# Kernel optimization log

Hardware: AMD Instinct MI355X
Metric: run time of the kernel (lower is better)

## Reference

```python
import jax, jax.numpy as jnp
import numpy as np

B, T, V, E, H, C = 64, 512, 32000, 256, 512, 4

def setup_inputs() -> dict:
    key = jax.random.key(0)
    ks = jax.random.split(key, 8)
    s = 1.0 / np.sqrt(H)  # torch LSTM default init scale
    return {
        "x": jax.random.randint(ks[0], (B, T), 0, V),
        "emb": jax.random.normal(ks[1], (V, E), jnp.float32) * 0.1,
        "W_ih": jax.random.uniform(ks[2], (4 * H, E), jnp.float32, -s, s),
        "W_hh": jax.random.uniform(ks[3], (4 * H, H), jnp.float32, -s, s),
        "b_ih": jax.random.uniform(ks[4], (4 * H,), jnp.float32, -s, s),
        "b_hh": jax.random.uniform(ks[5], (4 * H,), jnp.float32, -s, s),
        "W_fc": jax.random.uniform(ks[6], (C, H), jnp.float32, -s, s),
        "b_fc": jax.random.uniform(ks[7], (C,), jnp.float32, -s, s),
    }

def _lstm_last_hidden(e, W_ih, W_hh, b_ih, b_hh):
    # e: [B,T,E]. Precompute input-side gate preactivations for all steps.
    xg = jnp.einsum('bte,ge->tbg', e, W_ih) + (b_ih + b_hh)  # [T,B,4H]
    h0 = jnp.zeros((e.shape[0], H), e.dtype)
    c0 = jnp.zeros((e.shape[0], H), e.dtype)

    def step(carry, xt):
        h, c = carry
        g = xt + h @ W_hh.T                       # [B,4H]
        i, f, gg, o = jnp.split(g, 4, axis=-1)    # torch gate order: i,f,g,o
        i = jax.nn.sigmoid(i)
        f = jax.nn.sigmoid(f)
        gg = jnp.tanh(gg)
        o = jax.nn.sigmoid(o)
        c = f * c + i * gg
        h = o * jnp.tanh(c)
        return (h, c), None

    (hT, _), _ = jax.lax.scan(step, (h0, c0), xg)
    return hT  # last hidden == lstm_out[:, -1, :] for unidirectional LSTM

def reference(x, emb, W_ih, W_hh, b_ih, b_hh, W_fc, b_fc):
    e = emb[x]                                    # [B,T,E] embedding lookup
    hT = _lstm_last_hidden(e, W_ih, W_hh, b_ih, b_hh)
    return hT @ W_fc.T + b_fc                     # [B,C] logits
```

## Files before the change

kernel.cpp:

```cpp
#include <hip/hip_runtime.h>
#include <hip/hip_bf16.h>

#define B_  64
#define T_  512
#define E_  256
#define H_  512
#define G4_ 2048
#define C_  4

typedef __attribute__((ext_vector_type(4))) float  f32x4;
typedef __attribute__((ext_vector_type(8))) __bf16 bf16x8;
typedef __attribute__((ext_vector_type(8))) short  short8;
typedef __attribute__((ext_vector_type(4))) short  s16x4;

union V16 { f32x4 f; bf16x8 b; short8 s; };

__device__ __forceinline__ float sigmoid_(float x) { return 1.0f / (1.0f + __expf(-x)); }
__device__ __forceinline__ float tanh_(float x)    { return 1.0f - 2.0f / (__expf(2.0f * x) + 1.0f); }

__device__ __forceinline__ short f2bf(float f) {
  union { float f; unsigned u; } v; v.f = f;
  return (short)((v.u + 0x7FFFu + ((v.u >> 16) & 1u)) >> 16);
}

__device__ __forceinline__ void store_short_llc(void* p, unsigned v) {
  asm volatile("global_store_short %0, %1, off sc0 sc1" :: "v"(p), "v"(v) : "memory");
}
__device__ __forceinline__ void store_dword_llc(void* p, float v) {
  asm volatile("global_store_dword %0, %1, off sc0 sc1" :: "v"(p), "v"(v) : "memory");
}
__device__ __forceinline__ f32x4 ld_b128_llc(const void* p) {
  f32x4 v;
  asm volatile("global_load_dwordx4 %0, %1, off sc0 sc1\n\ts_waitcnt vmcnt(0)"
               : "=&v"(v) : "v"(p) : "memory");
  return v;
}

__global__ __launch_bounds__(256, 1) void wih_conv(const float* __restrict__ W,
                                                   short* __restrict__ out) {
  const int i = (blockIdx.x * 256 + threadIdx.x) * 4;
  f32x4 v = *(const f32x4*)(W + i);
  s16x4 s;
  s[0] = f2bf(v[0]); s[1] = f2bf(v[1]); s[2] = f2bf(v[2]); s[3] = f2bf(v[3]);
  *(s16x4*)(out + i) = s;
}

union XgSmem {
  struct { int idx[B_]; short e[B_][E_ + 8]; } g;
  short o[4][64][136];
};

template<bool WBF16>
__global__ __launch_bounds__(256, 2) void xg_kernel(
    const int* __restrict__ x, const float* __restrict__ emb,
    const void* __restrict__ Wv,
    __hip_bfloat16* __restrict__ xg)
{
  const int t   = blockIdx.x;
  const int tid = threadIdx.x;
  __shared__ XgSmem sm;

  if (tid < B_) sm.g.idx[tid] = x[tid * T_ + t];
  __syncthreads();
  {
    int b = tid >> 2, ch = tid & 3;
    const float* src = emb + (size_t)sm.g.idx[b] * E_ + ch * 64;
    short* dst = &sm.g.e[b][ch * 64];
#pragma unroll
    for (int i = 0; i < 16; i++) {
      f32x4 v = *(const f32x4*)(src + i * 4);
      s16x4 s;
      s[0] = f2bf(v[0]); s[1] = f2bf(v[1]); s[2] = f2bf(v[2]); s[3] = f2bf(v[3]);
      *(s16x4*)(dst + i * 4) = s;
    }
  }
  __syncthreads();

  const int wv   = tid >> 6;
  const int lane = tid & 63;
  const int ln15 = lane & 15, quad = lane >> 4;

  V16 breg[4][8];
#pragma unroll
  for (int nt = 0; nt < 4; nt++)
#pragma unroll
    for (int ks = 0; ks < 8; ks++)
      breg[nt][ks].f = *(const f32x4*)(&sm.g.e[nt * 16 + ln15][quad * 8 + ks * 32]);
  __syncthreads();

  const int gbase = wv * 512;
  const size_t base_t = (size_t)t * (G4_ * B_);

  for (int q = 0; q < 4; q++) {
#pragma unroll
    for (int m8 = 0; m8 < 8; m8++) {
      const int mt = q * 8 + m8;
      V16 areg[8];
      if constexpr (WBF16) {
        const short* arow = (const short*)Wv + (size_t)(gbase + mt * 16 + ln15) * E_ + quad * 8;
#pragma unroll
        for (int ks = 0; ks < 8; ks++)
          areg[ks].f = *(const f32x4*)(arow + ks * 32);
      } else {
        const float* arow = (const float*)Wv + (size_t)(gbase + mt * 16 + ln15) * E_ + quad * 8;
#pragma unroll
        for (int ks = 0; ks < 8; ks++) {
          f32x4 lo = *(const f32x4*)(arow + ks * 32);
          f32x4 hi = *(const f32x4*)(arow + ks * 32 + 4);
          short8 s;
          s[0] = f2bf(lo[0]); s[1] = f2bf(lo[1]); s[2] = f2bf(lo[2]); s[3] = f2bf(lo[3]);
          s[4] = f2bf(hi[0]); s[5] = f2bf(hi[1]); s[6] = f2bf(hi[2]); s[7] = f2bf(hi[3]);
          areg[ks].s = s;
        }
      }

      f32x4 acc[4];
#pragma unroll
      for (int nt = 0; nt < 4; nt++) acc[nt] = (f32x4){0.f, 0.f, 0.f, 0.f};
#pragma unroll
      for (int ks = 0; ks < 8; ks++)
#pragma unroll
        for (int nt = 0; nt < 4; nt++)
          acc[nt] = __builtin_amdgcn_mfma_f32_16x16x32_bf16(areg[ks].b, breg[nt][ks].b, acc[nt], 0, 0, 0);

      const int dl = m8 * 16 + quad * 4;
#pragma unroll
      for (int nt = 0; nt < 4; nt++) {
        const int batch = nt * 16 + ln15;
        s16x4 sv;
#pragma unroll
        for (int r = 0; r < 4; r++) sv[r] = f2bf(acc[nt][r]);
        *(s16x4*)&sm.o[wv][batch][dl] = sv;
      }
    }

    const size_t qbase = base_t + ((size_t)wv << 15) + q * 128;
    const int chunk = lane & 15;
#pragma unroll
    for (int i = 0; i < 16; i++) {
      const int row = (lane >> 4) + i * 4;
      f32x4 v = *(const f32x4*)&sm.o[wv][row][chunk * 8];
      *(f32x4*)((short*)xg + qbase + ((size_t)row << 9) + chunk * 8) = v;
    }
  }
}

__global__ __launch_bounds__(512, 2) void lstm_kernel(
    const float* __restrict__ W_hh,
    const float* __restrict__ b_ih, const float* __restrict__ b_hh,
    const float* __restrict__ W_fc, const float* __restrict__ b_fc,
    const __hip_bfloat16* __restrict__ xg,
    unsigned int* flags, __hip_bfloat16* hbuf , float* hT,
    float* out)
{
  const int tid  = threadIdx.x;
  const int blk  = blockIdx.x;
  const int g    = blk & 7;
  const int pd   = blk >> 3;
  const int d0   = pd * 64;
  const int wv   = tid >> 6;
  const int lane = tid & 63;
  const int ln15 = lane & 15, quad = lane >> 4;

  __shared__ __hip_bfloat16 s_h[16][520];
  __shared__ float s_pre[4][8][68];

  const int gate  = wv >> 1;
  const int dhalf = (wv & 1) * 32;
  V16 areg[2][16];
#pragma unroll
  for (int tau = 0; tau < 2; tau++) {
    const int grow = gate * 512 + d0 + dhalf + tau * 16 + ln15;
    const float* ap = W_hh + (size_t)grow * H_ + quad * 8;
#pragma unroll
    for (int ks = 0; ks < 16; ks++) {
      f32x4 lo = *(const f32x4*)(ap + ks * 32);
      f32x4 hi = *(const f32x4*)(ap + ks * 32 + 4);
      short8 s;
      s[0] = f2bf(lo[0]); s[1] = f2bf(lo[1]); s[2] = f2bf(lo[2]); s[3] = f2bf(lo[3]);
      s[4] = f2bf(hi[0]); s[5] = f2bf(hi[1]); s[6] = f2bf(hi[2]); s[7] = f2bf(hi[3]);
      areg[tau][ks].s = s;
    }
  }

  const int nb = tid >> 6;
  const int nd = tid & 63;
  const int gb = g * 8 + nb;
  const int dg = d0 + nd;
  const float bias_i = b_ih[dg]        + b_hh[dg];
  const float bias_f = b_ih[512 + dg]  + b_hh[512 + dg];
  const float bias_g = b_ih[1024 + dg] + b_hh[1024 + dg];
  const float bias_o = b_ih[1536 + dg] + b_hh[1536 + dg];
  float c = 0.0f;
  const int myflag = g * 16 + pd;

  *(f32x4*)&s_h[8 + (tid >> 6)][(tid & 63) * 8] = (f32x4){0.f, 0.f, 0.f, 0.f};

  for (int t = 0; t < T_; t++) {
    const int cur = t & 1, nxt = cur ^ 1;

    const size_t xoff = (size_t)t * (G4_ * B_) + ((size_t)gb << 9) + dg;
    const __hip_bfloat16 xgi = xg[xoff];
    const __hip_bfloat16 xgf = xg[xoff + (1u << 15)];
    const __hip_bfloat16 xgg = xg[xoff + (2u << 15)];
    const __hip_bfloat16 xgo = xg[xoff + (3u << 15)];

    if (tid < 8) {
      const unsigned* fp = flags + g * 16 + tid;
      while (__hip_atomic_load(fp, __ATOMIC_RELAXED, __HIP_MEMORY_SCOPE_AGENT) < (unsigned)t) {}
    }
    __syncthreads();

    {
      const short* hbase = (const short*)hbuf + (size_t)cur * (B_ * H_) + (size_t)(g * 8) * H_;
      f32x4 va = ld_b128_llc(hbase + tid * 8);
      *(f32x4*)&s_h[tid >> 6][(tid & 63) * 8] = va;
    }
    __syncthreads();

    f32x4 acc0 = (f32x4){0.f, 0.f, 0.f, 0.f};
    f32x4 acc1 = (f32x4){0.f, 0.f, 0.f, 0.f};
#pragma unroll
    for (int ks = 0; ks < 16; ks++) {
      V16 b0;
      b0.f = *(const f32x4*)&s_h[ln15][quad * 8 + ks * 32];
      acc0 = __builtin_amdgcn_mfma_f32_16x16x32_bf16(areg[0][ks].b, b0.b, acc0, 0, 0, 0);
      acc1 = __builtin_amdgcn_mfma_f32_16x16x32_bf16(areg[1][ks].b, b0.b, acc1, 0, 0, 0);
    }

    if (ln15 < 8) {
      *(f32x4*)&s_pre[gate][ln15][dhalf + quad * 4]      = acc0;
      *(f32x4*)&s_pre[gate][ln15][dhalf + 16 + quad * 4] = acc1;
    }
    __syncthreads();

    {
      const float pi = s_pre[0][nb][nd] + bias_i + __bfloat162float(xgi);
      const float pf = s_pre[1][nb][nd] + bias_f + __bfloat162float(xgf);
      const float pg = s_pre[2][nb][nd] + bias_g + __bfloat162float(xgg);
      const float po = s_pre[3][nb][nd] + bias_o + __bfloat162float(xgo);
      const float i_ = sigmoid_(pi), f_ = sigmoid_(pf);
      const float g_ = tanh_(pg),    o_ = sigmoid_(po);
      c = f_ * c + i_ * g_;
      const float h = o_ * tanh_(c);
      if (t < T_ - 1) {
        store_short_llc((short*)hbuf + (size_t)nxt * (B_ * H_) + (size_t)gb * H_ + dg,
                        (unsigned)(unsigned short)f2bf(h));
      } else {
        store_dword_llc(hT + gb * H_ + dg, h);
      }
    }
    __syncthreads();

    if (tid == 0)
      __hip_atomic_store(&flags[myflag], (unsigned)(t + 1),
                         __ATOMIC_RELAXED, __HIP_MEMORY_SCOPE_AGENT);
  }

  if (blk == 0) {
    if (tid < 64)
      while (__hip_atomic_load(flags + (tid >> 3) * 16 + (tid & 7),
                               __ATOMIC_RELAXED, __HIP_MEMORY_SCOPE_AGENT) < (unsigned)T_) {}
    __builtin_amdgcn_fence(__ATOMIC_ACQUIRE, "agent");
    __syncthreads();
    for (int o = tid; o < B_ * C_; o += 512) {
      const int b = o >> 2, cl = o & 3;
      const f32x4* hr = (const f32x4*)(hT + b * H_);
      const f32x4* wr = (const f32x4*)(W_fc + cl * H_);
      float s = 0.f;
      for (int d4 = 0; d4 < H_ / 4; d4++) {
        const f32x4 hv = hr[d4];
        const f32x4 wv4 = wr[d4];
        s += hv[0] * wv4[0] + hv[1] * wv4[1] + hv[2] * wv4[2] + hv[3] * wv4[3];
      }
      s += b_fc[cl];
      out[o] = s;
    }
  }
}

extern "C" void kernel_launch(void* const* d_in, const int* in_sizes, int n_in,
                              void* d_out, int out_size, void* d_ws, size_t ws_size,
                              hipStream_t stream) {
  const int*   x    = (const int*)d_in[0];
  const float* emb  = (const float*)d_in[1];
  const float* W_ih = (const float*)d_in[2];
  const float* W_hh = (const float*)d_in[3];
  const float* b_ih = (const float*)d_in[4];
  const float* b_hh = (const float*)d_in[5];
  const float* W_fc = (const float*)d_in[6];
  const float* b_fc = (const float*)d_in[7];
  float* out = (float*)d_out;

  char* ws = (char*)d_ws;
  const size_t XG_OFF  = 524288;
  const size_t XG_END  = XG_OFF + (size_t)T_ * G4_ * B_ * 2;
  const size_t NEEDED2 = XG_END + (size_t)G4_ * E_ * 2;
  if (ws_size < XG_END) return;

  unsigned int*   flags = (unsigned int*)ws;
  __hip_bfloat16* hbuf  = (__hip_bfloat16*)(ws + 4096);
  float*          hT    = (float*)(ws + 135168);
  __hip_bfloat16* xg    = (__hip_bfloat16*)(ws + XG_OFF);
  short*          wih16 = (short*)(ws + XG_END);

  (void)hipMemsetAsync(ws, 0, 135168, stream);

  if (ws_size >= NEEDED2) {
    wih_conv<<<512, 256, 0, stream>>>(W_ih, wih16);
    xg_kernel<true><<<T_, 256, 0, stream>>>(x, emb, wih16, xg);
  } else {
    xg_kernel<false><<<T_, 256, 0, stream>>>(x, emb, W_ih, xg);
  }
  lstm_kernel<<<64, 512, 0, stream>>>(W_hh, b_ih, b_hh, W_fc, b_fc, xg,
                                      flags, hbuf, hT, out);
}
```

Measured before the change: 1.263 ms.

## Replace per-step flag barriers with step-tagged hidden-state words and in-register gate math

Each hidden value is now stored as a 32-bit word that packs the step number with the bf16 value, so consumers spin on the data itself rather than on separate per-block flags. This drops the flag polling, the flag store and two block barriers per timestep. W_hh rows are reordered so each MFMA output lane holds all four gates for one unit, which lets the cell update run in registers without the shared-memory pre-activation exchange. The next step's xg values are prefetched, and a double-buffered LDS copy of h replaces one barrier. In exchange the hbuf traffic doubles in size, and every lane polls with repeated 128-bit loads, which adds load on the L2.

```diff
diff --git a/kernel.cpp b/kernel.cpp
--- a/kernel.cpp
+++ b/kernel.cpp
@@ -23,17 +23,17 @@
   return (short)((v.u + 0x7FFFu + ((v.u >> 16) & 1u)) >> 16);
 }
 
-__device__ __forceinline__ void store_short_llc(void* p, unsigned v) {
-  asm volatile("global_store_short %0, %1, off sc0 sc1" :: "v"(p), "v"(v) : "memory");
-}
-__device__ __forceinline__ void store_dword_llc(void* p, float v) {
+__device__ __forceinline__ void store_dword_llc_f(void* p, float v) {
   asm volatile("global_store_dword %0, %1, off sc0 sc1" :: "v"(p), "v"(v) : "memory");
 }
-__device__ __forceinline__ f32x4 ld_b128_llc(const void* p) {
-  f32x4 v;
-  asm volatile("global_load_dwordx4 %0, %1, off sc0 sc1\n\ts_waitcnt vmcnt(0)"
-               : "=&v"(v) : "v"(p) : "memory");
-  return v;
+__device__ __forceinline__ void store_dword_llc_u(void* p, unsigned v) {
+  asm volatile("global_store_dword %0, %1, off sc0 sc1" :: "v"(p), "v"(v) : "memory");
+}
+__device__ __forceinline__ void ld2_b128_llc(const void* p, f32x4& a, f32x4& b) {
+  asm volatile("global_load_dwordx4 %0, %2, off sc0 sc1\n\t"
+               "global_load_dwordx4 %1, %2, off offset:16 sc0 sc1\n\t"
+               "s_waitcnt vmcnt(0)"
+               : "=&v"(a), "=&v"(b) : "v"(p) : "memory");
 }
 
 __global__ __launch_bounds__(256, 1) void wih_conv(const float* __restrict__ W,
@@ -150,7 +150,7 @@
     const float* __restrict__ b_ih, const float* __restrict__ b_hh,
     const float* __restrict__ W_fc, const float* __restrict__ b_fc,
     const __hip_bfloat16* __restrict__ xg,
-    unsigned int* flags, __hip_bfloat16* hbuf , float* hT,
+    unsigned int* flags, unsigned int* hbuf , float* hT,
     float* out)
 {
   const int tid  = threadIdx.x;
@@ -162,15 +162,12 @@
   const int lane = tid & 63;
   const int ln15 = lane & 15, quad = lane >> 4;
 
-  __shared__ __hip_bfloat16 s_h[16][520];
-  __shared__ float s_pre[4][8][68];
-
-  const int gate  = wv >> 1;
-  const int dhalf = (wv & 1) * 32;
+  __shared__ __hip_bfloat16 s_h[2][16][520];
+
   V16 areg[2][16];
 #pragma unroll
   for (int tau = 0; tau < 2; tau++) {
-    const int grow = gate * 512 + d0 + dhalf + tau * 16 + ln15;
+    const int grow = (ln15 & 3) * 512 + d0 + wv * 8 + tau * 4 + (ln15 >> 2);
     const float* ap = W_hh + (size_t)grow * H_ + quad * 8;
 #pragma unroll
     for (int ks = 0; ks < 16; ks++) {
@@ -183,38 +180,61 @@
     }
   }
 
-  const int nb = tid >> 6;
-  const int nd = tid & 63;
-  const int gb = g * 8 + nb;
-  const int dg = d0 + nd;
-  const float bias_i = b_ih[dg]        + b_hh[dg];
-  const float bias_f = b_ih[512 + dg]  + b_hh[512 + dg];
-  const float bias_g = b_ih[1024 + dg] + b_hh[1024 + dg];
-  const float bias_o = b_ih[1536 + dg] + b_hh[1536 + dg];
-  float c = 0.0f;
-  const int myflag = g * 16 + pd;
-
-  *(f32x4*)&s_h[8 + (tid >> 6)][(tid & 63) * 8] = (f32x4){0.f, 0.f, 0.f, 0.f};
+  const int gb_ = g * 8 + ln15;
+  float bias[2][4];
+  float cst[2] = {0.f, 0.f};
+  __hip_bfloat16 xv[2][4];
+  if (ln15 < 8) {
+#pragma unroll
+    for (int tau = 0; tau < 2; tau++) {
+      const int dg_ = d0 + wv * 8 + tau * 4 + quad;
+#pragma unroll
+      for (int gg = 0; gg < 4; gg++)
+        bias[tau][gg] = b_ih[gg * 512 + dg_] + b_hh[gg * 512 + dg_];
+    }
+    const size_t xb = ((size_t)gb_ << 9);
+#pragma unroll
+    for (int tau = 0; tau < 2; tau++) {
+      const int dg_ = d0 + wv * 8 + tau * 4 + quad;
+#pragma unroll
+      for (int gg = 0; gg < 4; gg++)
+        xv[tau][gg] = xg[xb + ((size_t)gg << 15) + dg_];
+    }
+  }
+
+  *(f32x4*)&s_h[0][8 + wv][lane * 8] = (f32x4){0.f, 0.f, 0.f, 0.f};
+  *(f32x4*)&s_h[1][8 + wv][lane * 8] = (f32x4){0.f, 0.f, 0.f, 0.f};
+
+  const unsigned* hb0 = hbuf + ((size_t)(g * 8) << 9) + tid * 8;
+  const unsigned* hb1 = hb0 + B_ * H_;
+  unsigned* sb0 = hbuf + ((size_t)gb_ << 9);
+  unsigned* sb1 = sb0 + B_ * H_;
 
   for (int t = 0; t < T_; t++) {
-    const int cur = t & 1, nxt = cur ^ 1;
-
-    const size_t xoff = (size_t)t * (G4_ * B_) + ((size_t)gb << 9) + dg;
-    const __hip_bfloat16 xgi = xg[xoff];
-    const __hip_bfloat16 xgf = xg[xoff + (1u << 15)];
-    const __hip_bfloat16 xgg = xg[xoff + (2u << 15)];
-    const __hip_bfloat16 xgo = xg[xoff + (3u << 15)];
-
-    if (tid < 8) {
-      const unsigned* fp = flags + g * 16 + tid;
-      while (__hip_atomic_load(fp, __ATOMIC_RELAXED, __HIP_MEMORY_SCOPE_AGENT) < (unsigned)t) {}
-    }
-    __syncthreads();
-
     {
-      const short* hbase = (const short*)hbuf + (size_t)cur * (B_ * H_) + (size_t)(g * 8) * H_;
-      f32x4 va = ld_b128_llc(hbase + tid * 8);
-      *(f32x4*)&s_h[tid >> 6][(tid & 63) * 8] = va;
+      const unsigned want = (unsigned)t;
+      const unsigned* hb = (t & 1) ? hb1 : hb0;
+      f32x4 va, vb;
+      for (;;) {
+        ld2_b128_llc(hb, va, vb);
+        unsigned bad = 0;
+#pragma unroll
+        for (int i = 0; i < 4; i++) {
+          bad |= (__float_as_uint(va[i]) >> 16) ^ want;
+          bad |= (__float_as_uint(vb[i]) >> 16) ^ want;
+        }
+        if (!bad) break;
+      }
+      short8 sv;
+      sv[0] = (short)(__float_as_uint(va[0]) & 0xffffu);
+      sv[1] = (short)(__float_as_uint(va[1]) & 0xffffu);
+      sv[2] = (short)(__float_as_uint(va[2]) & 0xffffu);
+      sv[3] = (short)(__float_as_uint(va[3]) & 0xffffu);
+      sv[4] = (short)(__float_as_uint(vb[0]) & 0xffffu);
+      sv[5] = (short)(__float_as_uint(vb[1]) & 0xffffu);
+      sv[6] = (short)(__float_as_uint(vb[2]) & 0xffffu);
+      sv[7] = (short)(__float_as_uint(vb[3]) & 0xffffu);
+      *(short8*)&s_h[t & 1][tid >> 6][(tid & 63) * 8] = sv;
     }
     __syncthreads();
 
@@ -223,44 +243,55 @@
 #pragma unroll
     for (int ks = 0; ks < 16; ks++) {
       V16 b0;
-      b0.f = *(const f32x4*)&s_h[ln15][quad * 8 + ks * 32];
+      b0.f = *(const f32x4*)&s_h[t & 1][ln15][quad * 8 + ks * 32];
       acc0 = __builtin_amdgcn_mfma_f32_16x16x32_bf16(areg[0][ks].b, b0.b, acc0, 0, 0, 0);
       acc1 = __builtin_amdgcn_mfma_f32_16x16x32_bf16(areg[1][ks].b, b0.b, acc1, 0, 0, 0);
     }
 
     if (ln15 < 8) {
-      *(f32x4*)&s_pre[gate][ln15][dhalf + quad * 4]      = acc0;
-      *(f32x4*)&s_pre[gate][ln15][dhalf + 16 + quad * 4] = acc1;
-    }
-    __syncthreads();
-
-    {
-      const float pi = s_pre[0][nb][nd] + bias_i + __bfloat162float(xgi);
-      const float pf = s_pre[1][nb][nd] + bias_f + __bfloat162float(xgf);
-      const float pg = s_pre[2][nb][nd] + bias_g + __bfloat162float(xgg);
-      const float po = s_pre[3][nb][nd] + bias_o + __bfloat162float(xgo);
-      const float i_ = sigmoid_(pi), f_ = sigmoid_(pf);
-      const float g_ = tanh_(pg),    o_ = sigmoid_(po);
-      c = f_ * c + i_ * g_;
-      const float h = o_ * tanh_(c);
-      if (t < T_ - 1) {
-        store_short_llc((short*)hbuf + (size_t)nxt * (B_ * H_) + (size_t)gb * H_ + dg,
-                        (unsigned)(unsigned short)f2bf(h));
-      } else {
-        store_dword_llc(hT + gb * H_ + dg, h);
-      }
-    }
-    __syncthreads();
-
-    if (tid == 0)
-      __hip_atomic_store(&flags[myflag], (unsigned)(t + 1),
-                         __ATOMIC_RELAXED, __HIP_MEMORY_SCOPE_AGENT);
-  }
+      unsigned* sb = (t & 1) ? sb0 : sb1;
+#pragma unroll
+      for (int tau = 0; tau < 2; tau++) {
+        const f32x4 a = tau ? acc1 : acc0;
+        const float pi = a[0] + bias[tau][0] + __bfloat162float(xv[tau][0]);
+        const float pf = a[1] + bias[tau][1] + __bfloat162float(xv[tau][1]);
+        const float pg = a[2] + bias[tau][2] + __bfloat162float(xv[tau][2]);
+        const float po = a[3] + bias[tau][3] + __bfloat162float(xv[tau][3]);
+        const float i_ = sigmoid_(pi), f_ = sigmoid_(pf);
+        const float g_ = tanh_(pg),    o_ = sigmoid_(po);
+        cst[tau] = f_ * cst[tau] + i_ * g_;
+        const float h = o_ * tanh_(cst[tau]);
+        const int dg_ = d0 + wv * 8 + tau * 4 + quad;
+        if (t < T_ - 1) {
+          const unsigned pw = ((unsigned)(t + 1) << 16) | (unsigned)(unsigned short)f2bf(h);
+          store_dword_llc_u(sb + dg_, pw);
+        } else {
+          store_dword_llc_f(hT + gb_ * H_ + dg_, h);
+        }
+      }
+      if (t + 1 < T_) {
+        const size_t xb = (size_t)(t + 1) * (G4_ * B_) + ((size_t)gb_ << 9);
+#pragma unroll
+        for (int tau = 0; tau < 2; tau++) {
+          const int dg_ = d0 + wv * 8 + tau * 4 + quad;
+#pragma unroll
+          for (int gg = 0; gg < 4; gg++)
+            xv[tau][gg] = xg[xb + ((size_t)gg << 15) + dg_];
+        }
+      }
+    }
+  }
+
+  asm volatile("s_waitcnt vmcnt(0)" ::: "memory");
+  __syncthreads();
+  if (tid == 0)
+    __hip_atomic_store(&flags[g * 16 + pd], 1u,
+                       __ATOMIC_RELAXED, __HIP_MEMORY_SCOPE_AGENT);
 
   if (blk == 0) {
     if (tid < 64)
       while (__hip_atomic_load(flags + (tid >> 3) * 16 + (tid & 7),
-                               __ATOMIC_RELAXED, __HIP_MEMORY_SCOPE_AGENT) < (unsigned)T_) {}
+                               __ATOMIC_RELAXED, __HIP_MEMORY_SCOPE_AGENT) < 1u) {}
     __builtin_amdgcn_fence(__ATOMIC_ACQUIRE, "agent");
     __syncthreads();
     for (int o = tid; o < B_ * C_; o += 512) {
@@ -299,12 +330,12 @@
   if (ws_size < XG_END) return;
 
   unsigned int*   flags = (unsigned int*)ws;
-  __hip_bfloat16* hbuf  = (__hip_bfloat16*)(ws + 4096);
-  float*          hT    = (float*)(ws + 135168);
+  unsigned int*   hbuf  = (unsigned int*)(ws + 4096);
+  float*          hT    = (float*)(ws + 266240);
   __hip_bfloat16* xg    = (__hip_bfloat16*)(ws + XG_OFF);
   short*          wih16 = (short*)(ws + XG_END);
 
-  (void)hipMemsetAsync(ws, 0, 135168, stream);
+  (void)hipMemsetAsync(ws, 0, 266240, stream);
 
   if (ws_size >= NEEDED2) {
     wih_conv<<<512, 256, 0, stream>>>(W_ih, wih16);
```

After: 2.233 ms. 76.8% more time.

## Interleave gate rows in MFMA tiles to do cell update in registers

Applied to the files above, without the earlier changes.

Reorders the W_hh rows loaded into each wave's MFMA A-operand so that each 16-row tile holds the i,f,g,o gates for 4 hidden units side by side. Each lane's accumulator then already contains all four gate preactivations for one (batch, unit) pair. This removes the shared-memory staging buffer for preactivations and one block-wide barrier per timestep on the serial recurrence path. In exchange, only half the lanes (ln15<8) do the pointwise math, each handling two units, and the xg loads become scattered per lane.

```diff
diff --git a/kernel.cpp b/kernel.cpp
--- a/kernel.cpp
+++ b/kernel.cpp
@@ -163,14 +163,11 @@
   const int ln15 = lane & 15, quad = lane >> 4;
 
   __shared__ __hip_bfloat16 s_h[16][520];
-  __shared__ float s_pre[4][8][68];
-
-  const int gate  = wv >> 1;
-  const int dhalf = (wv & 1) * 32;
+
   V16 areg[2][16];
 #pragma unroll
   for (int tau = 0; tau < 2; tau++) {
-    const int grow = gate * 512 + d0 + dhalf + tau * 16 + ln15;
+    const int grow = (ln15 & 3) * 512 + d0 + wv * 8 + tau * 4 + (ln15 >> 2);
     const float* ap = W_hh + (size_t)grow * H_ + quad * 8;
 #pragma unroll
     for (int ks = 0; ks < 16; ks++) {
@@ -183,27 +180,37 @@
     }
   }
 
-  const int nb = tid >> 6;
-  const int nd = tid & 63;
-  const int gb = g * 8 + nb;
-  const int dg = d0 + nd;
-  const float bias_i = b_ih[dg]        + b_hh[dg];
-  const float bias_f = b_ih[512 + dg]  + b_hh[512 + dg];
-  const float bias_g = b_ih[1024 + dg] + b_hh[1024 + dg];
-  const float bias_o = b_ih[1536 + dg] + b_hh[1536 + dg];
-  float c = 0.0f;
+  const int gb_ = g * 8 + ln15;
+  float bias[2][4];
+  float cst[2] = {0.f, 0.f};
+  if (ln15 < 8) {
+#pragma unroll
+    for (int tau = 0; tau < 2; tau++) {
+      const int dg_ = d0 + wv * 8 + tau * 4 + quad;
+#pragma unroll
+      for (int gg = 0; gg < 4; gg++)
+        bias[tau][gg] = b_ih[gg * 512 + dg_] + b_hh[gg * 512 + dg_];
+    }
+  }
+
   const int myflag = g * 16 + pd;
 
-  *(f32x4*)&s_h[8 + (tid >> 6)][(tid & 63) * 8] = (f32x4){0.f, 0.f, 0.f, 0.f};
+  *(f32x4*)&s_h[8 + wv][lane * 8] = (f32x4){0.f, 0.f, 0.f, 0.f};
 
   for (int t = 0; t < T_; t++) {
     const int cur = t & 1, nxt = cur ^ 1;
 
-    const size_t xoff = (size_t)t * (G4_ * B_) + ((size_t)gb << 9) + dg;
-    const __hip_bfloat16 xgi = xg[xoff];
-    const __hip_bfloat16 xgf = xg[xoff + (1u << 15)];
-    const __hip_bfloat16 xgg = xg[xoff + (2u << 15)];
-    const __hip_bfloat16 xgo = xg[xoff + (3u << 15)];
+    __hip_bfloat16 xv[2][4];
+    if (ln15 < 8) {
+      const size_t xb = (size_t)t * (G4_ * B_) + ((size_t)gb_ << 9);
+#pragma unroll
+      for (int tau = 0; tau < 2; tau++) {
+        const int dg_ = d0 + wv * 8 + tau * 4 + quad;
+#pragma unroll
+        for (int gg = 0; gg < 4; gg++)
+          xv[tau][gg] = xg[xb + ((size_t)gg << 15) + dg_];
+      }
+    }
 
     if (tid < 8) {
       const unsigned* fp = flags + g * 16 + tid;
@@ -229,25 +236,23 @@
     }
 
     if (ln15 < 8) {
-      *(f32x4*)&s_pre[gate][ln15][dhalf + quad * 4]      = acc0;
-      *(f32x4*)&s_pre[gate][ln15][dhalf + 16 + quad * 4] = acc1;
-    }
-    __syncthreads();
-
-    {
-      const float pi = s_pre[0][nb][nd] + bias_i + __bfloat162float(xgi);
-      const float pf = s_pre[1][nb][nd] + bias_f + __bfloat162float(xgf);
-      const float pg = s_pre[2][nb][nd] + bias_g + __bfloat162float(xgg);
-      const float po = s_pre[3][nb][nd] + bias_o + __bfloat162float(xgo);
-      const float i_ = sigmoid_(pi), f_ = sigmoid_(pf);
-      const float g_ = tanh_(pg),    o_ = sigmoid_(po);
-      c = f_ * c + i_ * g_;
-      const float h = o_ * tanh_(c);
-      if (t < T_ - 1) {
-        store_short_llc((short*)hbuf + (size_t)nxt * (B_ * H_) + (size_t)gb * H_ + dg,
-                        (unsigned)(unsigned short)f2bf(h));
-      } else {
-        store_dword_llc(hT + gb * H_ + dg, h);
+      short* sb = (short*)hbuf + (size_t)nxt * (B_ * H_) + (size_t)gb_ * H_;
+#pragma unroll
+      for (int tau = 0; tau < 2; tau++) {
+        const f32x4 a = tau ? acc1 : acc0;
+        const float pi = a[0] + bias[tau][0] + __bfloat162float(xv[tau][0]);
+        const float pf = a[1] + bias[tau][1] + __bfloat162float(xv[tau][1]);
+        const float pg = a[2] + bias[tau][2] + __bfloat162float(xv[tau][2]);
+        const float po = a[3] + bias[tau][3] + __bfloat162float(xv[tau][3]);
+        const float i_ = sigmoid_(pi), f_ = sigmoid_(pf);
+        const float g_ = tanh_(pg),    o_ = sigmoid_(po);
+        cst[tau] = f_ * cst[tau] + i_ * g_;
+        const float h = o_ * tanh_(cst[tau]);
+        const int dg_ = d0 + wv * 8 + tau * 4 + quad;
+        if (t < T_ - 1)
+          store_short_llc(sb + dg_, (unsigned)(unsigned short)f2bf(h));
+        else
+          store_dword_llc(hT + gb_ * H_ + dg_, h);
       }
     }
     __syncthreads();
```

Measured after the change: 1.657 ms. 31.2% more time.

## Replace per-step flag barrier with timestamp-tagged hidden state polling

Applied to the files above, without the earlier changes.

Each hidden-state element is now stored as a 32-bit word with the step number in the upper 16 bits, and consumers spin on the data itself until every tag matches the current step. This removes the separate flag array, the per-step flag store, the extra __syncthreads before publishing, and the flag-spin plus barrier before loading. In exchange the hidden buffer doubles in size, each thread loads two 128-bit vectors per step, and correctness relies on each tagged dword store becoming visible atomically. Final completion is signalled once per block through a new flag array.

```diff
diff --git a/kernel.cpp b/kernel.cpp
--- a/kernel.cpp
+++ b/kernel.cpp
@@ -23,17 +23,17 @@
   return (short)((v.u + 0x7FFFu + ((v.u >> 16) & 1u)) >> 16);
 }
 
-__device__ __forceinline__ void store_short_llc(void* p, unsigned v) {
-  asm volatile("global_store_short %0, %1, off sc0 sc1" :: "v"(p), "v"(v) : "memory");
-}
-__device__ __forceinline__ void store_dword_llc(void* p, float v) {
+__device__ __forceinline__ void store_dword_llc_f(void* p, float v) {
   asm volatile("global_store_dword %0, %1, off sc0 sc1" :: "v"(p), "v"(v) : "memory");
 }
-__device__ __forceinline__ f32x4 ld_b128_llc(const void* p) {
-  f32x4 v;
-  asm volatile("global_load_dwordx4 %0, %1, off sc0 sc1\n\ts_waitcnt vmcnt(0)"
-               : "=&v"(v) : "v"(p) : "memory");
-  return v;
+__device__ __forceinline__ void store_dword_llc_u(void* p, unsigned v) {
+  asm volatile("global_store_dword %0, %1, off sc0 sc1" :: "v"(p), "v"(v) : "memory");
+}
+__device__ __forceinline__ void ld2_b128_llc(const void* p, f32x4& a, f32x4& b) {
+  asm volatile("global_load_dwordx4 %0, %2, off sc0 sc1\n\t"
+               "global_load_dwordx4 %1, %2, off offset:16 sc0 sc1\n\t"
+               "s_waitcnt vmcnt(0)"
+               : "=&v"(a), "=&v"(b) : "v"(p) : "memory");
 }
 
 __global__ __launch_bounds__(256, 1) void wih_conv(const float* __restrict__ W,
@@ -150,7 +150,7 @@
     const float* __restrict__ b_ih, const float* __restrict__ b_hh,
     const float* __restrict__ W_fc, const float* __restrict__ b_fc,
     const __hip_bfloat16* __restrict__ xg,
-    unsigned int* flags, __hip_bfloat16* hbuf , float* hT,
+    unsigned int* flags2, unsigned int* hbuf , float* hT,
     float* out)
 {
   const int tid  = threadIdx.x;
@@ -192,12 +192,14 @@
   const float bias_g = b_ih[1024 + dg] + b_hh[1024 + dg];
   const float bias_o = b_ih[1536 + dg] + b_hh[1536 + dg];
   float c = 0.0f;
-  const int myflag = g * 16 + pd;
-
-  *(f32x4*)&s_h[8 + (tid >> 6)][(tid & 63) * 8] = (f32x4){0.f, 0.f, 0.f, 0.f};
+
+  *(f32x4*)&s_h[8 + wv][lane * 8] = (f32x4){0.f, 0.f, 0.f, 0.f};
+
+  const unsigned* hb0 = hbuf + ((size_t)(g * 8) << 9) + tid * 8;
+  const unsigned* hb1 = hb0 + B_ * H_;
 
   for (int t = 0; t < T_; t++) {
-    const int cur = t & 1, nxt = cur ^ 1;
+    const int nxt = (t & 1) ^ 1;
 
     const size_t xoff = (size_t)t * (G4_ * B_) + ((size_t)gb << 9) + dg;
     const __hip_bfloat16 xgi = xg[xoff];
@@ -205,16 +207,30 @@
     const __hip_bfloat16 xgg = xg[xoff + (2u << 15)];
     const __hip_bfloat16 xgo = xg[xoff + (3u << 15)];
 
-    if (tid < 8) {
-      const unsigned* fp = flags + g * 16 + tid;
-      while (__hip_atomic_load(fp, __ATOMIC_RELAXED, __HIP_MEMORY_SCOPE_AGENT) < (unsigned)t) {}
-    }
-    __syncthreads();
-
     {
-      const short* hbase = (const short*)hbuf + (size_t)cur * (B_ * H_) + (size_t)(g * 8) * H_;
-      f32x4 va = ld_b128_llc(hbase + tid * 8);
-      *(f32x4*)&s_h[tid >> 6][(tid & 63) * 8] = va;
+      const unsigned want = (unsigned)t;
+      const unsigned* hb = (t & 1) ? hb1 : hb0;
+      f32x4 va, vb;
+      for (;;) {
+        ld2_b128_llc(hb, va, vb);
+        unsigned bad = 0;
+#pragma unroll
+        for (int i = 0; i < 4; i++) {
+          bad |= (__float_as_uint(va[i]) >> 16) ^ want;
+          bad |= (__float_as_uint(vb[i]) >> 16) ^ want;
+        }
+        if (!bad) break;
+      }
+      short8 sv;
+      sv[0] = (short)(__float_as_uint(va[0]) & 0xffffu);
+      sv[1] = (short)(__float_as_uint(va[1]) & 0xffffu);
+      sv[2] = (short)(__float_as_uint(va[2]) & 0xffffu);
+      sv[3] = (short)(__float_as_uint(va[3]) & 0xffffu);
+      sv[4] = (short)(__float_as_uint(vb[0]) & 0xffffu);
+      sv[5] = (short)(__float_as_uint(vb[1]) & 0xffffu);
+      sv[6] = (short)(__float_as_uint(vb[2]) & 0xffffu);
+      sv[7] = (short)(__float_as_uint(vb[3]) & 0xffffu);
+      *(short8*)&s_h[tid >> 6][(tid & 63) * 8] = sv;
     }
     __syncthreads();
 
@@ -244,23 +260,24 @@
       c = f_ * c + i_ * g_;
       const float h = o_ * tanh_(c);
       if (t < T_ - 1) {
-        store_short_llc((short*)hbuf + (size_t)nxt * (B_ * H_) + (size_t)gb * H_ + dg,
-                        (unsigned)(unsigned short)f2bf(h));
+        const unsigned pw = ((unsigned)(t + 1) << 16) | (unsigned)(unsigned short)f2bf(h);
+        store_dword_llc_u(hbuf + (size_t)nxt * (B_ * H_) + ((size_t)gb << 9) + dg, pw);
       } else {
-        store_dword_llc(hT + gb * H_ + dg, h);
-      }
-    }
-    __syncthreads();
-
-    if (tid == 0)
-      __hip_atomic_store(&flags[myflag], (unsigned)(t + 1),
-                         __ATOMIC_RELAXED, __HIP_MEMORY_SCOPE_AGENT);
-  }
+        store_dword_llc_f(hT + gb * H_ + dg, h);
+      }
+    }
+  }
+
+  asm volatile("s_waitcnt vmcnt(0)" ::: "memory");
+  __syncthreads();
+  if (tid == 0)
+    __hip_atomic_store(&flags2[blk], 1u,
+                       __ATOMIC_RELEASE, __HIP_MEMORY_SCOPE_AGENT);
 
   if (blk == 0) {
     if (tid < 64)
-      while (__hip_atomic_load(flags + (tid >> 3) * 16 + (tid & 7),
-                               __ATOMIC_RELAXED, __HIP_MEMORY_SCOPE_AGENT) < (unsigned)T_) {}
+      while (__hip_atomic_load(&flags2[tid],
+                               __ATOMIC_RELAXED, __HIP_MEMORY_SCOPE_AGENT) < 1u) {}
     __builtin_amdgcn_fence(__ATOMIC_ACQUIRE, "agent");
     __syncthreads();
     for (int o = tid; o < B_ * C_; o += 512) {
@@ -298,13 +315,14 @@
   const size_t NEEDED2 = XG_END + (size_t)G4_ * E_ * 2;
   if (ws_size < XG_END) return;
 
-  unsigned int*   flags = (unsigned int*)ws;
-  __hip_bfloat16* hbuf  = (__hip_bfloat16*)(ws + 4096);
-  float*          hT    = (float*)(ws + 135168);
-  __hip_bfloat16* xg    = (__hip_bfloat16*)(ws + XG_OFF);
-  short*          wih16 = (short*)(ws + XG_END);
-
-  (void)hipMemsetAsync(ws, 0, 135168, stream);
+  unsigned int*   ctl    = (unsigned int*)ws;
+  unsigned int*   flags2 = ctl + 256;
+  unsigned int*   hbuf   = (unsigned int*)(ws + 4096);
+  float*          hT     = (float*)(ws + 266240);
+  __hip_bfloat16* xg     = (__hip_bfloat16*)(ws + XG_OFF);
+  short*          wih16  = (short*)(ws + XG_END);
+
+  (void)hipMemsetAsync(ws, 0, 266240, stream);
 
   if (ws_size >= NEEDED2) {
     wih_conv<<<512, 256, 0, stream>>>(W_ih, wih16);
@@ -313,5 +331,5 @@
     xg_kernel<false><<<T_, 256, 0, stream>>>(x, emb, W_ih, xg);
   }
   lstm_kernel<<<64, 512, 0, stream>>>(W_hh, b_ih, b_hh, W_fc, b_fc, xg,
-                                      flags, hbuf, hT, out);
-}
+                                      flags2, hbuf, hT, out);
+}
```

After: 1.277 ms. No clear change (+1.1%).
